# Kernel tuning notes

Hardware: AMD Instinct MI355X
Metric: run time of the kernel (lower is better)

Reference implementation:

```python
import math
import jax, jax.numpy as jnp
import numpy as np

B, N, C, H = 64, 197, 768, 12
KEEP_RATE = 0.7

def setup_inputs() -> dict:
    key = jax.random.key(0)
    k0, k1, k2 = jax.random.split(key, 3)
    x = jax.random.normal(k0, (B, N, C), jnp.float32)
    qkv_w = jax.random.normal(k1, (C, 3 * C), jnp.float32) * 0.02
    qkv_b = jnp.zeros((3 * C,), jnp.float32)
    proj_w = jax.random.normal(k2, (C, C), jnp.float32) * 0.02
    proj_b = jnp.zeros((C,), jnp.float32)
    return {"x": x, "qkv_w": qkv_w, "qkv_b": qkv_b, "proj_w": proj_w, "proj_b": proj_b}

def reference(x, qkv_w, qkv_b, proj_w, proj_b):
    b, n, c = x.shape
    d = c // H
    scale = d ** -0.5
    # qkv: [B,N,3C] -> [3,B,H,N,d]
    qkv = (x @ qkv_w + qkv_b).reshape(b, n, 3, H, d)
    qkv = jnp.transpose(qkv, (2, 0, 3, 1, 4))
    q, k, v = qkv[0], qkv[1], qkv[2]
    attn = jax.nn.softmax(jnp.einsum('bhnd,bhmd->bhnm', q, k) * scale, axis=-1)  # [B,H,N,N]
    out = jnp.einsum('bhnm,bhmd->bhnd', attn, v)          # [B,H,N,d]
    out = jnp.transpose(out, (0, 2, 1, 3)).reshape(b, n, c)
    x_out = out @ proj_w + proj_b                          # [B,N,C]
    # dynamic token pruning via CLS attention (row 0, excluding CLS itself)
    left_tokens = math.ceil(KEEP_RATE * (n - 1))
    cls_attn = attn[:, :, 0, 1:].mean(axis=1)              # [B,N-1]
    _, idx = jax.lax.top_k(cls_attn, left_tokens)          # descending, sorted
    index = jnp.broadcast_to(idx[:, :, None], (b, left_tokens, c))
    return (x_out, index, idx, cls_attn, left_tokens)
```

## Files before the change

### kernel.cpp

```cpp
#include <hip/hip_runtime.h>
#include <math.h>

#define BB   64
#define NTOK 197
#define CC   768
#define HH   12
#define DH   64
#define MTOT (BB * NTOK)
#define MPAD 12672
#define LEFT 138

#define XOUT_OFF  0
#define INDEX_OFF 9682944
#define IDX_OFF   16465920
#define CLS_OFF   16474752
#define LT_OFF    16487296

typedef short s8v __attribute__((ext_vector_type(8)));
typedef short s4v __attribute__((ext_vector_type(4)));
typedef float f4v __attribute__((ext_vector_type(4)));

#define GLOAD16(g, l) __builtin_amdgcn_global_load_lds( \
    (const __attribute__((address_space(1))) unsigned int*)(g), \
    (__attribute__((address_space(3))) unsigned int*)(l), 16, 0, 0)

__device__ __forceinline__ unsigned short f2bf(float f) {
    union { float f; unsigned int i; } x; x.f = f;
    unsigned int r = x.i + 0x7FFFu + ((x.i >> 16) & 1u);
    return (unsigned short)(r >> 16);
}

__global__ __launch_bounds__(256)
void convert_x(const float* __restrict__ in, unsigned short* __restrict__ outb)
{
    size_t i = ((size_t)blockIdx.x * 256 + threadIdx.x) * 8;
    float4 a = *(const float4*)(in + i);
    float4 b = *(const float4*)(in + i + 4);
    s8v r;
    r[0] = (short)f2bf(a.x); r[1] = (short)f2bf(a.y);
    r[2] = (short)f2bf(a.z); r[3] = (short)f2bf(a.w);
    r[4] = (short)f2bf(b.x); r[5] = (short)f2bf(b.y);
    r[6] = (short)f2bf(b.z); r[7] = (short)f2bf(b.w);
    *(s8v*)(outb + i) = r;
}

__global__ __launch_bounds__(256)
void transpose_w(const float* __restrict__ in, unsigned short* __restrict__ outb, int N)
{
    __shared__ float tile[32][33];
    const int bi = blockIdx.x, bj = blockIdx.y;
    const int tx = threadIdx.x & 31, ty = threadIdx.x >> 5;
#pragma unroll
    for (int r = ty; r < 32; r += 8)
        tile[r][tx] = in[(size_t)(bi * 32 + r) * N + bj * 32 + tx];
    __syncthreads();
#pragma unroll
    for (int r = ty; r < 32; r += 8)
        outb[(size_t)(bj * 32 + r) * 768 + bi * 32 + tx] = f2bf(tile[tx][r]);
}

__global__ __launch_bounds__(256, 3)
void gemm_bf16(const unsigned short* __restrict__ A, const unsigned short* __restrict__ BT,
               const float* __restrict__ bias, int ncolt, int mode,
               unsigned short* __restrict__ outb, float* __restrict__ outf)
{
    const int id = blockIdx.x;
    const int xcd = id & 7;
    const int t = id >> 3;
    const int ct = t % ncolt, s = t / ncolt;
    const int rt = s * 8 + xcd;
    if (rt >= 99) return;
    const int m0 = rt * 128, n0 = ct * 128;

    const int tid = threadIdx.x;
    const int wave = tid >> 6, lane = tid & 63;
    const int quad = lane >> 4, l16 = lane & 15;
    const int rowbase = (wave >> 1) * 64, colbase = (wave & 1) * 64;
    __shared__ __align__(16) short As[128 * 64];
    __shared__ __align__(16) short Bs[128 * 64];

    const int rA   = lane >> 3;
    const int gcol = ((lane & 7) ^ rA) * 8;
    unsigned int agof[4], bgof[4];
#pragma unroll
    for (int i = 0; i < 4; ++i) {
        int c = wave * 4 + i;
        agof[i] = (unsigned int)((m0 + c * 8 + rA) * 768 + gcol);
        bgof[i] = (unsigned int)((n0 + c * 8 + rA) * 768 + gcol);
    }
    int aoff[4], boff[4];
#pragma unroll
    for (int i = 0; i < 4; ++i) {
        aoff[i] = (rowbase + i * 16 + l16) * 64 + ((quad ^ (l16 & 7)) * 8);
        boff[i] = (colbase + i * 16 + l16) * 64 + ((quad ^ (l16 & 7)) * 8);
    }

    f4v acc[4][4];
#pragma unroll
    for (int i = 0; i < 4; ++i)
#pragma unroll
        for (int j = 0; j < 4; ++j) acc[i][j] = (f4v)0.f;

    for (int k0 = 0; k0 < 768; k0 += 64) {
#pragma unroll
        for (int i = 0; i < 4; ++i) {
            int c = wave * 4 + i;
            GLOAD16(A  + agof[i] + k0, &As[c * 512]);
            GLOAD16(BT + bgof[i] + k0, &Bs[c * 512]);
        }
        __syncthreads();
#pragma unroll
        for (int ks = 0; ks < 2; ++ks) {
            const int x = ks * 32;
            s8v af[4], bf[4];
#pragma unroll
            for (int i = 0; i < 4; ++i) af[i] = *(const s8v*)&As[aoff[i] ^ x];
#pragma unroll
            for (int j = 0; j < 4; ++j) bf[j] = *(const s8v*)&Bs[boff[j] ^ x];
#pragma unroll
            for (int i = 0; i < 4; ++i)
#pragma unroll
                for (int j = 0; j < 4; ++j)
                    acc[i][j] = __builtin_amdgcn_mfma_f32_16x16x32_bf16(bf[j], af[i], acc[i][j], 0, 0, 0);
        }
        __syncthreads();
    }

    const int ncols = mode ? 768 : 2304;
#pragma unroll
    for (int i = 0; i < 4; ++i) {
        const int m = m0 + rowbase + i * 16 + l16;
        if (m >= MTOT) continue;
#pragma unroll
        for (int j = 0; j < 4; ++j) {
            const int nb = n0 + colbase + j * 16 + quad * 4;
            float4 b4 = *(const float4*)&bias[nb];
            if (mode == 1) {
                float4 r;
                r.x = acc[i][j][0] + b4.x; r.y = acc[i][j][1] + b4.y;
                r.z = acc[i][j][2] + b4.z; r.w = acc[i][j][3] + b4.w;
                *(float4*)(outf + (size_t)m * ncols + nb) = r;
            } else {
                s4v r;
                r[0] = (short)f2bf(acc[i][j][0] + b4.x);
                r[1] = (short)f2bf(acc[i][j][1] + b4.y);
                r[2] = (short)f2bf(acc[i][j][2] + b4.z);
                r[3] = (short)f2bf(acc[i][j][3] + b4.w);
                *(s4v*)(outb + (size_t)m * ncols + nb) = r;
            }
        }
    }
}

#define PSTR 228

__global__ __launch_bounds__(256)
void attn_mfma(const unsigned short* __restrict__ qkv, unsigned short* __restrict__ attnbf)
{
    const int bh = blockIdx.x;
    const int b = bh / HH, h = bh - b * HH;
    const int tid = threadIdx.x;
    const int wave = tid >> 6, lane = tid & 63;
    const int quad = lane >> 4, l16 = lane & 15;
    __shared__ short Vs[64 * PSTR];
    __shared__ short Ps[4][16 * PSTR];

    const unsigned short* qg = qkv + (size_t)b * NTOK * 2304 + h * DH;
    const unsigned short* kg = qg + 768;
    const unsigned short* vg = qg + 1536;

    if (tid < NTOK) {
#pragma unroll
        for (int c = 0; c < 8; ++c) {
            s8v vv = *(const s8v*)(vg + (size_t)tid * 2304 + c * 8);
#pragma unroll
            for (int e = 0; e < 8; ++e) Vs[(c * 8 + e) * PSTR + tid] = vv[e];
        }
    }
    for (int f = tid; f < 64 * (PSTR - NTOK); f += 256) {
        int dd = f / (PSTR - NTOK);
        int tk = NTOK + (f - dd * (PSTR - NTOK));
        Vs[dd * PSTR + tk] = 0;
    }
    __syncthreads();

    for (int strip = wave; strip < 13; strip += 4) {
        const int mq = min(strip * 16 + l16, NTOK - 1);
        const s8v aq0 = *(const s8v*)(qg + (size_t)mq * 2304 + quad * 8);
        const s8v aq1 = *(const s8v*)(qg + (size_t)mq * 2304 + 32 + quad * 8);

        f4v sacc[14];
#pragma unroll
        for (int j = 0; j < 14; ++j) sacc[j] = (f4v)0.f;
#pragma unroll
        for (int j = 0; j < 14; ++j) {
            const int kt = min(j * 16 + l16, NTOK - 1);
            s8v bk0 = *(const s8v*)(kg + (size_t)kt * 2304 + quad * 8);
            s8v bk1 = *(const s8v*)(kg + (size_t)kt * 2304 + 32 + quad * 8);
            sacc[j] = __builtin_amdgcn_mfma_f32_16x16x32_bf16(bk0, aq0, sacc[j], 0, 0, 0);
            sacc[j] = __builtin_amdgcn_mfma_f32_16x16x32_bf16(bk1, aq1, sacc[j], 0, 0, 0);
        }

        float mx = -1e30f;
#pragma unroll
        for (int j = 0; j < 14; ++j)
#pragma unroll
            for (int r = 0; r < 4; ++r) {
                const int key = j * 16 + quad * 4 + r;
                float s = (key < NTOK) ? sacc[j][r] * 0.125f : -1e30f;
                sacc[j][r] = s;
                mx = fmaxf(mx, s);
            }
        mx = fmaxf(mx, __shfl_xor(mx, 16, 64));
        mx = fmaxf(mx, __shfl_xor(mx, 32, 64));

        float sm = 0.f;
#pragma unroll
        for (int j = 0; j < 14; ++j) {
            s4v pk;
#pragma unroll
            for (int r = 0; r < 4; ++r) {
                const int key = j * 16 + quad * 4 + r;
                float p = (key < NTOK) ? __expf(sacc[j][r] - mx) : 0.f;
                sm += p;
                pk[r] = (short)f2bf(p);
            }
            *(s4v*)&Ps[wave][l16 * PSTR + j * 16 + quad * 4] = pk;
        }
        sm += __shfl_xor(sm, 16, 64);
        sm += __shfl_xor(sm, 32, 64);
        const float rcp = 1.f / sm;

        f4v oacc[4];
#pragma unroll
        for (int j = 0; j < 4; ++j) oacc[j] = (f4v)0.f;
#pragma unroll
        for (int t = 0; t < 7; ++t) {
            const int ko = t * 32 + quad * 8;
            s8v ap = *(const s8v*)&Ps[wave][l16 * PSTR + ko];
#pragma unroll
            for (int j = 0; j < 4; ++j) {
                s8v bv = *(const s8v*)&Vs[(j * 16 + l16) * PSTR + ko];
                oacc[j] = __builtin_amdgcn_mfma_f32_16x16x32_bf16(bv, ap, oacc[j], 0, 0, 0);
            }
        }
        const int qrow = strip * 16 + l16;
        if (qrow < NTOK) {
#pragma unroll
            for (int j = 0; j < 4; ++j) {
                s4v o4;
#pragma unroll
                for (int r = 0; r < 4; ++r) o4[r] = (short)f2bf(oacc[j][r] * rcp);
                *(s4v*)&attnbf[((size_t)b * NTOK + qrow) * 768 + h * DH + j * 16 + quad * 4] = o4;
            }
        }
    }
}

__global__ __launch_bounds__(256)
void qr_kernel(const float* __restrict__ x, const float* __restrict__ qkv_w,
               const float* __restrict__ qkv_b, float* __restrict__ rws,
               float* __restrict__ bconst)
{
    const int blk = blockIdx.x;
    const int b = blk / HH, h = blk - b * HH;
    const int tid = threadIdx.x;
    __shared__ float x0[CC];
    __shared__ float q0h[DH];
    for (int c = tid; c < CC; c += 256) x0[c] = x[(size_t)b * NTOK * CC + c];
    __syncthreads();
    if (tid < DH) {
        const int o = h * DH + tid;
        float acc = qkv_b[o];
        for (int c = 0; c < CC; ++c)
            acc = fmaf(x0[c], qkv_w[(size_t)c * 2304 + o], acc);
        q0h[tid] = acc;
    }
    __syncthreads();
    for (int c = tid; c < CC; c += 256) {
        const float* wrow = qkv_w + (size_t)c * 2304 + CC + h * DH;
        float acc = 0.f;
#pragma unroll
        for (int d = 0; d < DH; d += 4) {
            float4 w4 = *(const float4*)(wrow + d);
            acc = fmaf(w4.x, q0h[d + 0], acc);
            acc = fmaf(w4.y, q0h[d + 1], acc);
            acc = fmaf(w4.z, q0h[d + 2], acc);
            acc = fmaf(w4.w, q0h[d + 3], acc);
        }
        rws[((size_t)b * HH + h) * CC + c] = acc;
    }
    if (tid == 0) {
        float acc = 0.f;
        for (int d = 0; d < DH; ++d) acc += q0h[d] * qkv_b[CC + h * DH + d];
        bconst[blk] = acc;
    }
}

__global__ __launch_bounds__(256)
void cls_s(const float* __restrict__ x, const float* __restrict__ rws,
           const float* __restrict__ bconst, float* __restrict__ sws)
{
    const int b = blockIdx.x;
    const int tid = threadIdx.x;
    __shared__ __align__(16) float rl[HH][CC];
    __shared__ float bcs[HH];
    for (int u = tid; u < HH * CC; u += 256)
        ((float*)rl)[u] = rws[(size_t)b * HH * CC + u];
    if (tid < HH) bcs[tid] = bconst[b * HH + tid];
    __syncthreads();
    if (tid < NTOK) {
        const float* xr = x + ((size_t)b * NTOK + tid) * CC;
        float acc[HH];
#pragma unroll
        for (int h = 0; h < HH; ++h) acc[h] = 0.f;
        for (int c = 0; c < CC; c += 4) {
            float4 x4 = *(const float4*)(xr + c);
#pragma unroll
            for (int h = 0; h < HH; ++h) {
                float4 r4 = *(const float4*)&rl[h][c];
                acc[h] = fmaf(x4.x, r4.x, acc[h]);
                acc[h] = fmaf(x4.y, r4.y, acc[h]);
                acc[h] = fmaf(x4.z, r4.z, acc[h]);
                acc[h] = fmaf(x4.w, r4.w, acc[h]);
            }
        }
#pragma unroll
        for (int h = 0; h < HH; ++h)
            sws[((size_t)b * HH + h) * NTOK + tid] = (acc[h] + bcs[h]) * 0.125f;
    }
}

__global__ __launch_bounds__(256)
void cls_topk(const float* __restrict__ sws, float* __restrict__ out, int write_lt)
{
    const int b = blockIdx.x, tid = threadIdx.x;
    const int wave = tid >> 6, lane = tid & 63;
    __shared__ float sbuf[HH][208];
    __shared__ float pm[4][208];
    __shared__ float vals[256];
    __shared__ int   idxs[256];

    for (int jj = lane; jj < 208; jj += 64) pm[wave][jj] = 0.f;
    if (tid < NTOK) {
#pragma unroll
        for (int h = 0; h < HH; ++h)
            sbuf[h][tid] = sws[((size_t)b * HH + h) * NTOK + tid];
    }
    __syncthreads();

    for (int h = wave; h < HH; h += 4) {
        float sv[4], ev[4];
        float mx = -1e30f;
#pragma unroll
        for (int t = 0; t < 4; ++t) {
            int j = lane + 64 * t;
            sv[t] = (j < NTOK) ? sbuf[h][j] : -1e30f;
            mx = fmaxf(mx, sv[t]);
        }
#pragma unroll
        for (int off = 1; off < 64; off <<= 1) mx = fmaxf(mx, __shfl_xor(mx, off, 64));
        float sm = 0.f;
#pragma unroll
        for (int t = 0; t < 4; ++t) {
            int j = lane + 64 * t;
            ev[t] = (j < NTOK) ? expf(sv[t] - mx) : 0.f;
            sm += ev[t];
        }
#pragma unroll
        for (int off = 1; off < 64; off <<= 1) sm += __shfl_xor(sm, off, 64);
#pragma unroll
        for (int t = 0; t < 4; ++t) {
            int j = lane + 64 * t;
            if (j < NTOK) pm[wave][j] += ev[t] / sm;
        }
    }
    __syncthreads();

    float v = -INFINITY;
    int id = 256 + tid;
    if (tid < NTOK - 1) {
        int j = tid + 1;
        float s = ((pm[0][j] + pm[1][j]) + (pm[2][j] + pm[3][j])) * (1.f / 12.f);
        v = s; id = tid;
        out[CLS_OFF + (size_t)b * (NTOK - 1) + tid] = s;
    }
    vals[tid] = v; idxs[tid] = id;
    __syncthreads();

    for (int k = 2; k <= 256; k <<= 1) {
        for (int j = k >> 1; j > 0; j >>= 1) {
            int ixj = tid ^ j;
            if (ixj > tid) {
                float va = vals[tid], vb2 = vals[ixj];
                int ia = idxs[tid], ib = idxs[ixj];
                bool aLess = (va > vb2) || (va == vb2 && ia < ib);
                bool dir = ((tid & k) == 0);
                if (dir != aLess) {
                    vals[tid] = vb2; vals[ixj] = va;
                    idxs[tid] = ib;  idxs[ixj] = ia;
                }
            }
            __syncthreads();
        }
    }

    if (tid < LEFT) out[IDX_OFF + (size_t)b * LEFT + tid] = (float)idxs[tid];
    for (int u = tid; u < LEFT * CC; u += 256) {
        int t = u / CC;
        out[INDEX_OFF + (size_t)b * LEFT * CC + u] = (float)idxs[t];
    }
    if (write_lt && b == 0 && tid == 0) out[LT_OFF] = (float)LEFT;
}

extern "C" void kernel_launch(void* const* d_in, const int* in_sizes, int n_in,
                              void* d_out, int out_size, void* d_ws, size_t ws_size,
                              hipStream_t stream)
{
    const float* x      = (const float*)d_in[0];
    const float* qkv_w  = (const float*)d_in[1];
    const float* qkv_b  = (const float*)d_in[2];
    const float* proj_w = (const float*)d_in[3];
    const float* proj_b = (const float*)d_in[4];
    float* out = (float*)d_out;

    char* w = (char*)d_ws;
    unsigned short* xbf   = (unsigned short*)w; w += (size_t)MPAD * CC * 2;
    unsigned short* wt1   = (unsigned short*)w; w += (size_t)3 * CC * CC * 2;
    unsigned short* wt2   = (unsigned short*)w; w += (size_t)CC * CC * 2;
    unsigned short* qkvbf = (unsigned short*)w; w += (size_t)MTOT * 3 * CC * 2;
    unsigned short* atbf  = (unsigned short*)w; w += (size_t)MPAD * CC * 2;
    float* rws    = (float*)w; w += (size_t)BB * HH * CC * 4;
    float* bconst = (float*)w; w += (size_t)BB * HH * 4;
    float* sws    = (float*)w; w += (size_t)BB * HH * NTOK * 4;

    convert_x<<<dim3(4728), 256, 0, stream>>>(x, xbf);
    transpose_w<<<dim3(24, 72), 256, 0, stream>>>(qkv_w, wt1, 3 * CC);
    transpose_w<<<dim3(24, 24), 256, 0, stream>>>(proj_w, wt2, CC);
    gemm_bf16<<<dim3(8 * 18 * 13), 256, 0, stream>>>(xbf, wt1, qkv_b, 18, 0, qkvbf, nullptr);
    attn_mfma<<<dim3(BB * HH), 256, 0, stream>>>(qkvbf, atbf);
    gemm_bf16<<<dim3(8 * 6 * 13), 256, 0, stream>>>(atbf, wt2, proj_b, 6, 1,
                                                    nullptr, out + XOUT_OFF);
    qr_kernel<<<dim3(BB * HH), 256, 0, stream>>>(x, qkv_w, qkv_b, rws, bconst);
    cls_s<<<dim3(BB), 256, 0, stream>>>(x, rws, bconst, sws);
    cls_topk<<<dim3(BB), 256, 0, stream>>>(sws, out, (out_size > LT_OFF) ? 1 : 0);
}
```

Before: 386.8 us.

## Parallelize CLS score kernel over token-head pairs across more blocks

The cls_s kernel previously used one block per batch, with each of 197 threads computing all 12 head dot products. It now launches 10 blocks per batch, one thread per (token, head) pair, and pads the shared rows to 772 floats to reduce LDS bank conflicts. This raises parallelism from 64 blocks to 640 to fill more CUs. In exchange, each x row is read from global memory 12 times (once per head, mostly hitting cache), and every block reloads the full rws slice into shared memory.

```diff
diff --git a/kernel.cpp b/kernel.cpp
--- a/kernel.cpp
+++ b/kernel.cpp
@@ -301,33 +301,32 @@
 void cls_s(const float* __restrict__ x, const float* __restrict__ rws,
            const float* __restrict__ bconst, float* __restrict__ sws)
 {
-    const int b = blockIdx.x;
+    const int b = blockIdx.y;
     const int tid = threadIdx.x;
-    __shared__ __align__(16) float rl[HH][CC];
+    __shared__ __align__(16) float rl[HH * 772];
     __shared__ float bcs[HH];
-    for (int u = tid; u < HH * CC; u += 256)
-        ((float*)rl)[u] = rws[(size_t)b * HH * CC + u];
+#pragma unroll
+    for (int h = 0; h < HH; ++h)
+        for (int c = tid; c < CC; c += 256)
+            rl[h * 772 + c] = rws[((size_t)b * HH + h) * CC + c];
     if (tid < HH) bcs[tid] = bconst[b * HH + tid];
     __syncthreads();
-    if (tid < NTOK) {
-        const float* xr = x + ((size_t)b * NTOK + tid) * CC;
-        float acc[HH];
-#pragma unroll
-        for (int h = 0; h < HH; ++h) acc[h] = 0.f;
+    const int local = blockIdx.x * 256 + tid;
+    if (local < NTOK * HH) {
+        const int tok = local / HH;
+        const int h = local - tok * HH;
+        const float* xr = x + ((size_t)b * NTOK + tok) * CC;
+        const float* rp = rl + h * 772;
+        float acc = 0.f;
         for (int c = 0; c < CC; c += 4) {
             float4 x4 = *(const float4*)(xr + c);
-#pragma unroll
-            for (int h = 0; h < HH; ++h) {
-                float4 r4 = *(const float4*)&rl[h][c];
-                acc[h] = fmaf(x4.x, r4.x, acc[h]);
-                acc[h] = fmaf(x4.y, r4.y, acc[h]);
-                acc[h] = fmaf(x4.z, r4.z, acc[h]);
-                acc[h] = fmaf(x4.w, r4.w, acc[h]);
-            }
-        }
-#pragma unroll
-        for (int h = 0; h < HH; ++h)
-            sws[((size_t)b * HH + h) * NTOK + tid] = (acc[h] + bcs[h]) * 0.125f;
+            float4 r4 = *(const float4*)(rp + c);
+            acc = fmaf(x4.x, r4.x, acc);
+            acc = fmaf(x4.y, r4.y, acc);
+            acc = fmaf(x4.z, r4.z, acc);
+            acc = fmaf(x4.w, r4.w, acc);
+        }
+        sws[((size_t)b * HH + h) * NTOK + tok] = (acc + bcs[h]) * 0.125f;
     }
 }
 
@@ -442,6 +441,6 @@
     gemm_bf16<<<dim3(8 * 6 * 13), 256, 0, stream>>>(atbf, wt2, proj_b, 6, 1,
                                                     nullptr, out + XOUT_OFF);
     qr_kernel<<<dim3(BB * HH), 256, 0, stream>>>(x, qkv_w, qkv_b, rws, bconst);
-    cls_s<<<dim3(BB), 256, 0, stream>>>(x, rws, bconst, sws);
+    cls_s<<<dim3(10, 64), 256, 0, stream>>>(x, rws, bconst, sws);
     cls_topk<<<dim3(BB), 256, 0, stream>>>(sws, out, (out_size > LT_OFF) ? 1 : 0);
 }
```

After: 349.6 us. 9.6% less time.
